# Kernel tuning notes

Hardware: AMD Instinct MI355X
Metric: run time of the kernel (lower is better)

The kernel has to match this reference:

```python
import jax, jax.numpy as jnp
import numpy as np

B, S, D, H = 8, 512, 1024, 16
DK = D // H


def setup_inputs() -> dict:
    key = jax.random.key(0)
    ks = jax.random.split(key, 12)
    inp = {
        "input_Q": jax.random.normal(ks[0], (B, S, D), jnp.float32),
        "input_K": jax.random.normal(ks[1], (B, S, D), jnp.float32),
        "input_V": jax.random.normal(ks[2], (B, S, D), jnp.float32),
        "attn_mask": jax.random.bernoulli(ks[3], 0.1, (B, S, S)),
        "adj_matrix": jax.random.uniform(ks[4], (B, S, S), jnp.float32),
        "dist_matrix": jax.random.uniform(ks[5], (B, S, S), jnp.float32) * 5.0,
        # learned params (nn.Linear weights are [out, in], no bias)
        "W_Q": jax.random.normal(ks[6], (D, D), jnp.float32) / np.sqrt(D),
        "W_K": jax.random.normal(ks[7], (D, D), jnp.float32) / np.sqrt(D),
        "W_V": jax.random.normal(ks[8], (D, D), jnp.float32) / np.sqrt(D),
        "W_fc": jax.random.normal(ks[9], (D, D), jnp.float32) / np.sqrt(D),
        # Conv2d(3->1, k=1): weight [1,3,1,1] flattened to [3], bias [1]
        "conv_w": jax.random.normal(ks[10], (3,), jnp.float32) * 0.3,
        "conv_b": jax.random.normal(ks[11], (1,), jnp.float32) * 0.1,
    }
    return inp


def reference(input_Q, input_K, input_V, attn_mask, adj_matrix, dist_matrix,
              W_Q, W_K, W_V, W_fc, conv_w, conv_b):
    neg = jnp.float32(-1e9)
    # projections -> [B, H, S, dk]
    def proj(x, W):
        return jnp.einsum('bsd,od->bso', x, W).reshape(B, S, H, DK).transpose(0, 2, 1, 3)
    Q = proj(input_Q, W_Q)
    K = proj(input_K, W_K)
    V = proj(input_V, W_V)

    mask4 = attn_mask[:, None]  # [B,1,S,S] broadcast over heads
    # distance kernel: exp(-d), masked positions -> exp(-inf)=0
    dist_k = jnp.where(attn_mask, 0.0, jnp.exp(-dist_matrix))[:, None]  # [B,1,S,S]
    adj4 = adj_matrix[:, None]

    scores = jnp.einsum('bhqd,bhkd->bhqk', Q, K) / np.sqrt(DK).astype(np.float32)
    scores = jnp.where(mask4, neg, scores)
    scores = jax.nn.softmax(scores, axis=-1)

    # 1x1 conv over channels {scores, dist, adj}
    weighted = conv_w[0] * scores + conv_w[1] * dist_k + conv_w[2] * adj4 + conv_b[0]
    weighted = jnp.where(mask4, neg, weighted)
    attn = jax.nn.softmax(weighted, axis=-1)

    context = jnp.einsum('bhqk,bhkd->bhqd', attn, V)
    context = context.transpose(0, 2, 1, 3).reshape(B, S, D)
    output = jnp.einsum('bsd,od->bso', context, W_fc)
    return (output, attn)
```

## Files before the change

kernel.cpp:

```cpp
#include <hip/hip_runtime.h>
#include <stdint.h>

#define B_ 8
#define S_ 512
#define D_ 1024
#define H_ 16
#define DK_ 64

typedef float f32x4 __attribute__((ext_vector_type(4)));
typedef float float4v __attribute__((ext_vector_type(4)));
typedef short bf16x8 __attribute__((ext_vector_type(8)));
typedef short short4v __attribute__((ext_vector_type(4)));
typedef __bf16 bfv8 __attribute__((ext_vector_type(8)));

__device__ __forceinline__ short f2bf(float f) {
    uint32_t u = __builtin_bit_cast(uint32_t, f);
    u += 0x7FFFu + ((u >> 16) & 1u);
    return (short)(uint16_t)(u >> 16);
}

__device__ __forceinline__ f32x4 mfma_bf16(bf16x8 a, bf16x8 b, f32x4 c) {
    return __builtin_amdgcn_mfma_f32_16x16x32_bf16(
        __builtin_bit_cast(bfv8, a), __builtin_bit_cast(bfv8, b), c, 0, 0, 0);
}

__device__ __forceinline__ bf16x8 pack8(float4v a, float4v b) {
    bf16x8 v;
    v[0] = f2bf(a[0]); v[1] = f2bf(a[1]); v[2] = f2bf(a[2]); v[3] = f2bf(a[3]);
    v[4] = f2bf(b[0]); v[5] = f2bf(b[1]); v[6] = f2bf(b[2]); v[7] = f2bf(b[3]);
    return v;
}

__global__ __launch_bounds__(256) void precomp_kernel(
    const int* __restrict__ mask, const float* __restrict__ adj,
    const float* __restrict__ dist, const float* __restrict__ cw,
    const float* __restrict__ cb, float* __restrict__ comb, int n)
{
    const float w1 = cw[1], w2 = cw[2], b0 = cb[0];
    for (int i = blockIdx.x * 256 + threadIdx.x; i < n; i += gridDim.x * 256) {
        float c = -1e9f;
        if (mask[i] == 0) c = fmaf(w2, adj[i], fmaf(w1, __expf(-dist[i]), b0));
        comb[i] = c;
    }
}

__global__ __launch_bounds__(256) void proj_qkv_kernel(
    const float* __restrict__ xq, const float* __restrict__ xk, const float* __restrict__ xv,
    const float* __restrict__ wqp, const float* __restrict__ wkp, const float* __restrict__ wvp,
    short* __restrict__ Qp, short* __restrict__ Kp, short* __restrict__ VpT)
{
    __shared__ __align__(16) short Alds[128 * 64];
    __shared__ __align__(16) short Blds[128 * 64];

    const int z = blockIdx.z;
    const float* X = (z == 0) ? xq : (z == 1) ? xk : xv;
    const float* W = (z == 0) ? wqp : (z == 1) ? wkp : wvp;

    const int tid = threadIdx.x;
    const int lane = tid & 63, wid = tid >> 6;
    const int l15 = lane & 15, lg = lane >> 4;
    const int m0 = blockIdx.y * 128, n0 = blockIdx.x * 128;
    const int wm = wid >> 1, wn = wid & 1;

    f32x4 acc[4][4] = {};

    for (int k0 = 0; k0 < D_; k0 += 64) {
        #pragma unroll
        for (int g = 0; g < 4; ++g) {
            const int c = g * 256 + tid;
            const int row = c >> 3, cc = c & 7;
            const int swc = cc ^ (row & 7);
            const float* ga = X + (size_t)(m0 + row) * D_ + k0 + cc * 8;
            float4v a0 = *(const float4v*)ga;
            float4v a1 = *(const float4v*)(ga + 4);
            *(bf16x8*)&Alds[(row * 8 + swc) * 8] = pack8(a0, a1);
            const float* gb = W + (size_t)(n0 + row) * D_ + k0 + cc * 8;
            float4v b0v = *(const float4v*)gb;
            float4v b1v = *(const float4v*)(gb + 4);
            *(bf16x8*)&Blds[(row * 8 + swc) * 8] = pack8(b0v, b1v);
        }
        __syncthreads();
        #pragma unroll
        for (int ks = 0; ks < 2; ++ks) {
            bf16x8 af[4], bfr[4];
            #pragma unroll
            for (int i = 0; i < 4; ++i) {
                const int row = wm * 64 + i * 16 + l15;
                af[i] = *(const bf16x8*)&Alds[(row * 8 + ((ks * 4 + lg) ^ (row & 7))) * 8];
            }
            #pragma unroll
            for (int j = 0; j < 4; ++j) {
                const int row = wn * 64 + j * 16 + l15;
                bfr[j] = *(const bf16x8*)&Blds[(row * 8 + ((ks * 4 + lg) ^ (row & 7))) * 8];
            }
            #pragma unroll
            for (int i = 0; i < 4; ++i)
                #pragma unroll
                for (int j = 0; j < 4; ++j)
                    acc[i][j] = mfma_bf16(af[i], bfr[j], acc[i][j]);
        }
        __syncthreads();
    }

    if (z < 2) {
        short* Outp = (z == 0) ? Qp : Kp;
        #pragma unroll
        for (int i = 0; i < 4; ++i) {
            #pragma unroll
            for (int j = 0; j < 4; ++j) {
                const int n = n0 + wn * 64 + j * 16 + l15;
                const int h = n >> 6, dk = n & 63;
                #pragma unroll
                for (int r = 0; r < 4; ++r) {
                    const int m = m0 + wm * 64 + i * 16 + lg * 4 + r;
                    const int b = m >> 9, s = m & 511;
                    Outp[((size_t)(b * H_ + h) * S_ + s) * DK_ + dk] = f2bf(acc[i][j][r]);
                }
            }
        }
    } else {
        #pragma unroll
        for (int i = 0; i < 4; ++i) {
            const int mb = m0 + wm * 64 + i * 16 + lg * 4;
            const int b = mb >> 9, s0v = mb & 511;
            #pragma unroll
            for (int j = 0; j < 4; ++j) {
                const int n = n0 + wn * 64 + j * 16 + l15;
                const int h = n >> 6, dk = n & 63;
                short4v v;
                #pragma unroll
                for (int r = 0; r < 4; ++r) v[r] = f2bf(acc[i][j][r]);
                *(short4v*)&VpT[((size_t)(b * H_ + h) * DK_ + dk) * S_ + s0v] = v;
            }
        }
    }
}

__global__ __launch_bounds__(256, 4) void attn_kernel(
    const short* __restrict__ Qp, const short* __restrict__ Kp,
    const short* __restrict__ VpT, const float* __restrict__ comb,
    const float* __restrict__ cw, float* __restrict__ attn_out,
    short* __restrict__ Ctx)
{
    __shared__ __align__(16) char smem[16 * 1024 + 1024];
    float* red = (float*)(smem + 16384);

    const int tid = threadIdx.x;
    const int lane = tid & 63, w = tid >> 6;
    const int l15 = lane & 15, lg = lane >> 4;

    const int id = blockIdx.x;
    const int b = id & 7;
    const int rest = id >> 3;
    const int qt = rest & 31, h = rest >> 5;
    const int bh = b * H_ + h;
    const int q0 = qt * 16;
    const int k0 = w * 128;

    const short* Qb = Qp + (size_t)bh * S_ * DK_;
    const short* Kb = Kp + (size_t)bh * S_ * DK_ + (size_t)k0 * DK_;
    const short* Vb = VpT + (size_t)bh * DK_ * S_;
    const float* cbm = comb + (size_t)b * S_ * S_ + (size_t)q0 * S_ + k0;
    const float w0 = cw[0];

    bf16x8 aq0 = *(const bf16x8*)(Qb + (q0 + l15) * DK_ + lg * 8);
    bf16x8 aq1 = *(const bf16x8*)(Qb + (q0 + l15) * DK_ + 32 + lg * 8);

    f32x4 cmb[8];
    #pragma unroll
    for (int nf = 0; nf < 8; ++nf)
        #pragma unroll
        for (int r = 0; r < 4; ++r)
            cmb[nf][r] = cbm[(size_t)(lg * 4 + r) * S_ + nf * 16 + l15];

    f32x4 sc[8];
    #pragma unroll
    for (int nf = 0; nf < 8; ++nf) {
        bf16x8 bk0 = *(const bf16x8*)(Kb + (nf * 16 + l15) * DK_ + lg * 8);
        bf16x8 bk1 = *(const bf16x8*)(Kb + (nf * 16 + l15) * DK_ + 32 + lg * 8);
        f32x4 a = {};
        a = mfma_bf16(aq0, bk0, a);
        a = mfma_bf16(aq1, bk1, a);
        sc[nf] = a;
    }

    f32x4 mx;
    mx[0] = mx[1] = mx[2] = mx[3] = -3e38f;
    #pragma unroll
    for (int nf = 0; nf < 8; ++nf)
        #pragma unroll
        for (int r = 0; r < 4; ++r) {
            const float v = (cmb[nf][r] < -1e8f) ? -1e9f : sc[nf][r] * 0.125f;
            sc[nf][r] = v;
            mx[r] = fmaxf(mx[r], v);
        }
    #pragma unroll
    for (int off = 1; off < 16; off <<= 1)
        #pragma unroll
        for (int r = 0; r < 4; ++r)
            mx[r] = fmaxf(mx[r], __shfl_xor(mx[r], off));
    {
        float* rd = red;
        if (l15 == 0) {
            #pragma unroll
            for (int r = 0; r < 4; ++r) rd[w * 16 + lg * 4 + r] = mx[r];
        }
        __syncthreads();
        #pragma unroll
        for (int r = 0; r < 4; ++r) {
            const int row = lg * 4 + r;
            mx[r] = fmaxf(fmaxf(rd[row], rd[16 + row]), fmaxf(rd[32 + row], rd[48 + row]));
        }
    }

    f32x4 sm = {};
    #pragma unroll
    for (int nf = 0; nf < 8; ++nf)
        #pragma unroll
        for (int r = 0; r < 4; ++r) {
            const float e = __expf(sc[nf][r] - mx[r]);
            sc[nf][r] = e;
            sm[r] += e;
        }
    #pragma unroll
    for (int off = 1; off < 16; off <<= 1)
        #pragma unroll
        for (int r = 0; r < 4; ++r)
            sm[r] += __shfl_xor(sm[r], off);
    {
        float* rd = red + 64;
        if (l15 == 0) {
            #pragma unroll
            for (int r = 0; r < 4; ++r) rd[w * 16 + lg * 4 + r] = sm[r];
        }
        __syncthreads();
        #pragma unroll
        for (int r = 0; r < 4; ++r) {
            const int row = lg * 4 + r;
            sm[r] = (rd[row] + rd[16 + row]) + (rd[32 + row] + rd[48 + row]);
        }
    }
    f32x4 rs1;
    #pragma unroll
    for (int r = 0; r < 4; ++r) rs1[r] = 1.0f / sm[r];

    f32x4 mx2;
    mx2[0] = mx2[1] = mx2[2] = mx2[3] = -3e38f;
    #pragma unroll
    for (int nf = 0; nf < 8; ++nf)
        #pragma unroll
        for (int r = 0; r < 4; ++r) {
            const float p = sc[nf][r] * rs1[r];
            const float wv = fmaf(w0, p, cmb[nf][r]);
            sc[nf][r] = wv;
            mx2[r] = fmaxf(mx2[r], wv);
        }
    #pragma unroll
    for (int off = 1; off < 16; off <<= 1)
        #pragma unroll
        for (int r = 0; r < 4; ++r)
            mx2[r] = fmaxf(mx2[r], __shfl_xor(mx2[r], off));
    {
        float* rd = red + 128;
        if (l15 == 0) {
            #pragma unroll
            for (int r = 0; r < 4; ++r) rd[w * 16 + lg * 4 + r] = mx2[r];
        }
        __syncthreads();
        #pragma unroll
        for (int r = 0; r < 4; ++r) {
            const int row = lg * 4 + r;
            mx2[r] = fmaxf(fmaxf(rd[row], rd[16 + row]), fmaxf(rd[32 + row], rd[48 + row]));
        }
    }

    f32x4 sm2 = {};
    #pragma unroll
    for (int nf = 0; nf < 8; ++nf)
        #pragma unroll
        for (int r = 0; r < 4; ++r) {
            const float e = __expf(sc[nf][r] - mx2[r]);
            sc[nf][r] = e;
            sm2[r] += e;
        }
    #pragma unroll
    for (int off = 1; off < 16; off <<= 1)
        #pragma unroll
        for (int r = 0; r < 4; ++r)
            sm2[r] += __shfl_xor(sm2[r], off);
    {
        float* rd = red + 192;
        if (l15 == 0) {
            #pragma unroll
            for (int r = 0; r < 4; ++r) rd[w * 16 + lg * 4 + r] = sm2[r];
        }
        __syncthreads();
        #pragma unroll
        for (int r = 0; r < 4; ++r) {
            const int row = lg * 4 + r;
            sm2[r] = (rd[row] + rd[16 + row]) + (rd[32 + row] + rd[48 + row]);
        }
    }
    f32x4 rs2;
    #pragma unroll
    for (int r = 0; r < 4; ++r) rs2[r] = 1.0f / sm2[r];

    float* aout = attn_out + ((size_t)bh * S_ + q0) * S_ + k0;
    #pragma unroll
    for (int nf = 0; nf < 8; ++nf)
        #pragma unroll
        for (int r = 0; r < 4; ++r) {
            const int q = lg * 4 + r;
            const float av = sc[nf][r] * rs2[r];
            aout[(size_t)q * S_ + nf * 16 + l15] = av;
            const int byteo = ((q * 256 + (nf * 16 + l15) * 2) ^ ((q & 7) << 4)) + w * 4096;
            *(short*)(smem + byteo) = f2bf(av);
        }
    __syncthreads();

    f32x4 cacc[4] = {};
    #pragma unroll
    for (int ks = 0; ks < 4; ++ks) {
        const int byteA = ((l15 * 256 + (ks * 32 + lg * 8) * 2) ^ ((l15 & 7) << 4)) + w * 4096;
        bf16x8 pa = *(const bf16x8*)(smem + byteA);
        #pragma unroll
        for (int j = 0; j < 4; ++j) {
            bf16x8 bv = *(const bf16x8*)(Vb + (size_t)(j * 16 + l15) * S_ + k0 + ks * 32 + lg * 8);
            cacc[j] = mfma_bf16(pa, bv, cacc[j]);
        }
    }
    __syncthreads();

    float* cr = (float*)smem;
    #pragma unroll
    for (int j = 0; j < 4; ++j)
        #pragma unroll
        for (int r = 0; r < 4; ++r)
            cr[w * 1024 + (lg * 4 + r) * 64 + j * 16 + l15] = cacc[j][r];
    __syncthreads();

    #pragma unroll
    for (int r = 0; r < 4; ++r) {
        const int row = lg * 4 + r;
        const float v = (cr[row * 64 + w * 16 + l15] + cr[1024 + row * 64 + w * 16 + l15])
                      + (cr[2048 + row * 64 + w * 16 + l15] + cr[3072 + row * 64 + w * 16 + l15]);
        Ctx[(size_t)(b * S_ + q0 + row) * D_ + h * 64 + w * 16 + l15] = f2bf(v);
    }
}

__global__ __launch_bounds__(256) void fc_kernel(
    const short* __restrict__ Ctx, const float* __restrict__ Wfc,
    float* __restrict__ Out)
{
    __shared__ __align__(16) short Alds[128 * 64];
    __shared__ __align__(16) short Blds[128 * 64];

    const int tid = threadIdx.x;
    const int lane = tid & 63, wid = tid >> 6;
    const int l15 = lane & 15, lg = lane >> 4;
    const int m0 = blockIdx.y * 128, n0 = blockIdx.x * 128;
    const int wm = wid >> 1, wn = wid & 1;

    f32x4 acc[4][4] = {};

    for (int k0 = 0; k0 < D_; k0 += 64) {
        #pragma unroll
        for (int g = 0; g < 4; ++g) {
            const int c = g * 256 + tid;
            const int row = c >> 3, cc = c & 7;
            const int swc = cc ^ (row & 7);
            bf16x8 va = *(const bf16x8*)(Ctx + (size_t)(m0 + row) * D_ + k0 + cc * 8);
            *(bf16x8*)&Alds[(row * 8 + swc) * 8] = va;
            const float* gb = Wfc + (size_t)(n0 + row) * D_ + k0 + cc * 8;
            float4v b0v = *(const float4v*)gb;
            float4v b1v = *(const float4v*)(gb + 4);
            *(bf16x8*)&Blds[(row * 8 + swc) * 8] = pack8(b0v, b1v);
        }
        __syncthreads();
        #pragma unroll
        for (int ks = 0; ks < 2; ++ks) {
            bf16x8 af[4], bfr[4];
            #pragma unroll
            for (int i = 0; i < 4; ++i) {
                const int row = wm * 64 + i * 16 + l15;
                af[i] = *(const bf16x8*)&Alds[(row * 8 + ((ks * 4 + lg) ^ (row & 7))) * 8];
            }
            #pragma unroll
            for (int j = 0; j < 4; ++j) {
                const int row = wn * 64 + j * 16 + l15;
                bfr[j] = *(const bf16x8*)&Blds[(row * 8 + ((ks * 4 + lg) ^ (row & 7))) * 8];
            }
            #pragma unroll
            for (int i = 0; i < 4; ++i)
                #pragma unroll
                for (int j = 0; j < 4; ++j)
                    acc[i][j] = mfma_bf16(af[i], bfr[j], acc[i][j]);
        }
        __syncthreads();
    }

    #pragma unroll
    for (int i = 0; i < 4; ++i)
        #pragma unroll
        for (int j = 0; j < 4; ++j)
            #pragma unroll
            for (int r = 0; r < 4; ++r) {
                const int m = m0 + wm * 64 + i * 16 + lg * 4 + r;
                const int n = n0 + wn * 64 + j * 16 + l15;
                Out[(size_t)m * D_ + n] = acc[i][j][r];
            }
}

extern "C" void kernel_launch(void* const* d_in, const int* in_sizes, int n_in,
                              void* d_out, int out_size, void* d_ws, size_t ws_size,
                              hipStream_t stream) {
    const float* xq   = (const float*)d_in[0];
    const float* xk   = (const float*)d_in[1];
    const float* xv   = (const float*)d_in[2];
    const int*   mask = (const int*)d_in[3];
    const float* adj  = (const float*)d_in[4];
    const float* dist = (const float*)d_in[5];
    const float* wq   = (const float*)d_in[6];
    const float* wk   = (const float*)d_in[7];
    const float* wv   = (const float*)d_in[8];
    const float* wfc  = (const float*)d_in[9];
    const float* cw   = (const float*)d_in[10];
    const float* cb   = (const float*)d_in[11];

    float* out  = (float*)d_out;
    float* attn = out + (size_t)B_ * S_ * D_;

    char* ws = (char*)d_ws;
    short* Qp   = (short*)(ws);
    short* Kp   = (short*)(ws + (8u  << 20));
    short* VpT  = (short*)(ws + (16u << 20));
    short* Ctx  = (short*)(ws + (24u << 20));
    float* comb = (float*)(ws + (32u << 20));

    precomp_kernel<<<dim3(1024), dim3(256), 0, stream>>>(
        mask, adj, dist, cw, cb, comb, B_ * S_ * S_);
    proj_qkv_kernel<<<dim3(8, 32, 3), dim3(256), 0, stream>>>(
        xq, xk, xv, wq, wk, wv, Qp, Kp, VpT);
    attn_kernel<<<dim3(4096), dim3(256), 0, stream>>>(
        Qp, Kp, VpT, comb, cw, attn, Ctx);
    fc_kernel<<<dim3(8, 32), dim3(256), 0, stream>>>(Ctx, wfc, out);
}
```

Before: 213.2 us.

## Pre-convert inputs and weights to bf16, stage GEMM tiles via global_load_lds

Adds a separate kernel that converts X inputs and all weight matrices to bf16 once per call. The projection and fc GEMMs then copy tiles directly into LDS with global_load_lds instead of loading fp32 into registers and converting per tile. Block indices are remapped for better L2 reuse, and the workspace is reordered so comb aliases the Xb buffer after projection. This trades an extra full pass over the fp32 inputs (about 64MB read plus a bf16 write) for cheaper and simpler GEMM loads.

```diff
diff --git a/kernel.cpp b/kernel.cpp
--- a/kernel.cpp
+++ b/kernel.cpp
@@ -14,9 +14,7 @@
 typedef __bf16 bfv8 __attribute__((ext_vector_type(8)));
 
 __device__ __forceinline__ short f2bf(float f) {
-    uint32_t u = __builtin_bit_cast(uint32_t, f);
-    u += 0x7FFFu + ((u >> 16) & 1u);
-    return (short)(uint16_t)(u >> 16);
+    return __builtin_bit_cast(short, (__bf16)f);
 }
 
 __device__ __forceinline__ f32x4 mfma_bf16(bf16x8 a, bf16x8 b, f32x4 c) {
@@ -24,11 +22,44 @@
         __builtin_bit_cast(bfv8, a), __builtin_bit_cast(bfv8, b), c, 0, 0, 0);
 }
 
-__device__ __forceinline__ bf16x8 pack8(float4v a, float4v b) {
+__device__ __forceinline__ bf16x8 cvt8(float4v a, float4v b) {
     bf16x8 v;
     v[0] = f2bf(a[0]); v[1] = f2bf(a[1]); v[2] = f2bf(a[2]); v[3] = f2bf(a[3]);
     v[4] = f2bf(b[0]); v[5] = f2bf(b[1]); v[6] = f2bf(b[2]); v[7] = f2bf(b[3]);
     return v;
+}
+
+__device__ __forceinline__ void gl_lds16(const void* g, void* l) {
+    __builtin_amdgcn_global_load_lds(
+        (const __attribute__((address_space(1))) void*)g,
+        (__attribute__((address_space(3))) void*)l, 16, 0, 0);
+}
+
+__global__ __launch_bounds__(256) void conv_all_kernel(
+    const float* __restrict__ xq, const float* __restrict__ xk, const float* __restrict__ xv,
+    const float* __restrict__ wq, const float* __restrict__ wk, const float* __restrict__ wv,
+    const float* __restrict__ wfc, short* __restrict__ Xb, short* __restrict__ Wb)
+{
+    const int NX = 3 * 4096 * 1024;
+    const int NTOT = NX + 4 * 1024 * 1024;
+    for (int i = blockIdx.x * 256 + threadIdx.x; i * 8 < NTOT; i += gridDim.x * 256) {
+        const int i8 = i * 8;
+        const float* src;
+        short* dst;
+        if (i8 < NX) {
+            const int z = i8 >> 22, off = i8 & ((1 << 22) - 1);
+            src = ((z == 0) ? xq : (z == 1) ? xk : xv) + off;
+            dst = Xb + i8;
+        } else {
+            const int j = i8 - NX;
+            const int w = j >> 20, off = j & ((1 << 20) - 1);
+            src = ((w == 0) ? wq : (w == 1) ? wk : (w == 2) ? wv : wfc) + off;
+            dst = Wb + i8 - NX;
+        }
+        float4v a = *(const float4v*)src;
+        float4v b = *(const float4v*)(src + 4);
+        *(bf16x8*)dst = cvt8(a, b);
+    }
 }
 
 __global__ __launch_bounds__(256) void precomp_kernel(
@@ -45,39 +76,35 @@
 }
 
 __global__ __launch_bounds__(256) void proj_qkv_kernel(
-    const float* __restrict__ xq, const float* __restrict__ xk, const float* __restrict__ xv,
-    const float* __restrict__ wqp, const float* __restrict__ wkp, const float* __restrict__ wvp,
+    const short* __restrict__ Xb, const short* __restrict__ Wb,
     short* __restrict__ Qp, short* __restrict__ Kp, short* __restrict__ VpT)
 {
     __shared__ __align__(16) short Alds[128 * 64];
     __shared__ __align__(16) short Blds[128 * 64];
 
     const int z = blockIdx.z;
-    const float* X = (z == 0) ? xq : (z == 1) ? xk : xv;
-    const float* W = (z == 0) ? wqp : (z == 1) ? wkp : wvp;
+    const short* X = Xb + (size_t)z * (4096 * 1024);
+    const short* W = Wb + (size_t)z * (1024 * 1024);
 
     const int tid = threadIdx.x;
-    const int lane = tid & 63, wid = tid >> 6;
+    const int lane = tid & 63, w = tid >> 6;
     const int l15 = lane & 15, lg = lane >> 4;
-    const int m0 = blockIdx.y * 128, n0 = blockIdx.x * 128;
-    const int wm = wid >> 1, wn = wid & 1;
+
+    const int p = blockIdx.x;
+    const int lin = (p & 7) * 32 + (p >> 3);
+    const int n0 = (lin & 7) * 128, m0 = (lin >> 3) * 128;
+    const int wm = w >> 1, wn = w & 1;
 
     f32x4 acc[4][4] = {};
 
     for (int k0 = 0; k0 < D_; k0 += 64) {
         #pragma unroll
-        for (int g = 0; g < 4; ++g) {
-            const int c = g * 256 + tid;
-            const int row = c >> 3, cc = c & 7;
-            const int swc = cc ^ (row & 7);
-            const float* ga = X + (size_t)(m0 + row) * D_ + k0 + cc * 8;
-            float4v a0 = *(const float4v*)ga;
-            float4v a1 = *(const float4v*)(ga + 4);
-            *(bf16x8*)&Alds[(row * 8 + swc) * 8] = pack8(a0, a1);
-            const float* gb = W + (size_t)(n0 + row) * D_ + k0 + cc * 8;
-            float4v b0v = *(const float4v*)gb;
-            float4v b1v = *(const float4v*)(gb + 4);
-            *(bf16x8*)&Blds[(row * 8 + swc) * 8] = pack8(b0v, b1v);
+        for (int t = 0; t < 4; ++t) {
+            const int r0 = w * 32 + t * 8;
+            const int row = r0 + (lane >> 3);
+            const int sc = (lane & 7) ^ (row & 7);
+            gl_lds16(X + (size_t)(m0 + row) * D_ + k0 + sc * 8, &Alds[r0 * 64]);
+            gl_lds16(W + (size_t)(n0 + row) * D_ + k0 + sc * 8, &Blds[r0 * 64]);
         }
         __syncthreads();
         #pragma unroll
@@ -250,8 +277,8 @@
     for (int nf = 0; nf < 8; ++nf)
         #pragma unroll
         for (int r = 0; r < 4; ++r) {
-            const float p = sc[nf][r] * rs1[r];
-            const float wv = fmaf(w0, p, cmb[nf][r]);
+            const float pv = sc[nf][r] * rs1[r];
+            const float wv = fmaf(w0, pv, cmb[nf][r]);
             sc[nf][r] = wv;
             mx2[r] = fmaxf(mx2[r], wv);
         }
@@ -349,32 +376,31 @@
 }
 
 __global__ __launch_bounds__(256) void fc_kernel(
-    const short* __restrict__ Ctx, const float* __restrict__ Wfc,
+    const short* __restrict__ Ctx, const short* __restrict__ Wfcb,
     float* __restrict__ Out)
 {
     __shared__ __align__(16) short Alds[128 * 64];
     __shared__ __align__(16) short Blds[128 * 64];
 
     const int tid = threadIdx.x;
-    const int lane = tid & 63, wid = tid >> 6;
+    const int lane = tid & 63, w = tid >> 6;
     const int l15 = lane & 15, lg = lane >> 4;
-    const int m0 = blockIdx.y * 128, n0 = blockIdx.x * 128;
-    const int wm = wid >> 1, wn = wid & 1;
+
+    const int p = blockIdx.x;
+    const int lin = (p & 7) * 32 + (p >> 3);
+    const int n0 = (lin & 7) * 128, m0 = (lin >> 3) * 128;
+    const int wm = w >> 1, wn = w & 1;
 
     f32x4 acc[4][4] = {};
 
     for (int k0 = 0; k0 < D_; k0 += 64) {
         #pragma unroll
-        for (int g = 0; g < 4; ++g) {
-            const int c = g * 256 + tid;
-            const int row = c >> 3, cc = c & 7;
-            const int swc = cc ^ (row & 7);
-            bf16x8 va = *(const bf16x8*)(Ctx + (size_t)(m0 + row) * D_ + k0 + cc * 8);
-            *(bf16x8*)&Alds[(row * 8 + swc) * 8] = va;
-            const float* gb = Wfc + (size_t)(n0 + row) * D_ + k0 + cc * 8;
-            float4v b0v = *(const float4v*)gb;
-            float4v b1v = *(const float4v*)(gb + 4);
-            *(bf16x8*)&Blds[(row * 8 + swc) * 8] = pack8(b0v, b1v);
+        for (int t = 0; t < 4; ++t) {
+            const int r0 = w * 32 + t * 8;
+            const int row = r0 + (lane >> 3);
+            const int sc = (lane & 7) ^ (row & 7);
+            gl_lds16(Ctx + (size_t)(m0 + row) * D_ + k0 + sc * 8, &Alds[r0 * 64]);
+            gl_lds16(Wfcb + (size_t)(n0 + row) * D_ + k0 + sc * 8, &Blds[r0 * 64]);
         }
         __syncthreads();
         #pragma unroll
@@ -431,17 +457,22 @@
     float* attn = out + (size_t)B_ * S_ * D_;
 
     char* ws = (char*)d_ws;
-    short* Qp   = (short*)(ws);
-    short* Kp   = (short*)(ws + (8u  << 20));
-    short* VpT  = (short*)(ws + (16u << 20));
-    short* Ctx  = (short*)(ws + (24u << 20));
-    float* comb = (float*)(ws + (32u << 20));
-
+    short* Xb   = (short*)(ws);
+    float* comb = (float*)(ws);
+    short* Ctx  = (short*)(ws + (9u << 20));
+    short* Wb   = (short*)(ws + (24u << 20));
+    short* Qp   = (short*)(ws + (32u << 20));
+    short* Kp   = (short*)(ws + (40u << 20));
+    short* VpT  = (short*)(ws + (48u << 20));
+    const short* Wfcb = Wb + (size_t)3 * 1024 * 1024;
+
+    conv_all_kernel<<<dim3(2048), dim3(256), 0, stream>>>(
+        xq, xk, xv, wq, wk, wv, wfc, Xb, Wb);
+    proj_qkv_kernel<<<dim3(256, 1, 3), dim3(256), 0, stream>>>(
+        Xb, Wb, Qp, Kp, VpT);
     precomp_kernel<<<dim3(1024), dim3(256), 0, stream>>>(
         mask, adj, dist, cw, cb, comb, B_ * S_ * S_);
-    proj_qkv_kernel<<<dim3(8, 32, 3), dim3(256), 0, stream>>>(
-        xq, xk, xv, wq, wk, wv, Qp, Kp, VpT);
     attn_kernel<<<dim3(4096), dim3(256), 0, stream>>>(
         Qp, Kp, VpT, comb, cw, attn, Ctx);
-    fc_kernel<<<dim3(8, 32), dim3(256), 0, stream>>>(Ctx, wfc, out);
-}
+    fc_kernel<<<dim3(256), dim3(256), 0, stream>>>(Ctx, Wfcb, out);
+}
```

Result: faster. 174.4 us (-18.2%).
